# Optimization experiments

Hardware: AMD Instinct MI355X
Metric: run time of the kernel (lower is better)

## Reference

```python
import jax, jax.numpy as jnp
import numpy as np

R = 32  # voxel resolution


def _swish(x):
    return x * jax.nn.sigmoid(x)


def _group_norm(x, gamma, beta, groups, eps=1e-5):
    B, C = x.shape[0], x.shape[1]
    xr = x.reshape(B, groups, -1)
    mean = xr.mean(-1, keepdims=True)
    var = xr.var(-1, keepdims=True)
    xn = ((xr - mean) * jax.lax.rsqrt(var + eps)).reshape(x.shape)
    bshape = (1, C) + (1,) * (x.ndim - 2)
    return xn * gamma.reshape(bshape) + beta.reshape(bshape)


def _conv3d_same(x, w, b):
    # x: [B,C,D,H,W], w: [O,I,k,k,k], SAME padding (k//2)
    k = w.shape[-1]
    p = k // 2
    y = jax.lax.conv_general_dilated(
        x, w, window_strides=(1, 1, 1), padding=[(p, p)] * 3,
        dimension_numbers=('NCDHW', 'OIDHW', 'NCDHW'))
    return y + b[None, :, None, None, None]


def setup_inputs() -> dict:
    key = jax.random.key(0)
    ks = jax.random.split(key, 8)
    B, Cin, Cout, N = 8, 64, 128, 16384
    return {
        'features': jax.random.normal(ks[0], (B, Cin, N), jnp.float32),
        'coords': jax.random.normal(ks[1], (B, 3, N), jnp.float32),
        'temb': jnp.zeros((1,), jnp.float32),
        'w1': jax.random.normal(ks[2], (Cout, Cin, 3, 3, 3), jnp.float32) * 0.02,
        'b1': jnp.zeros((Cout,), jnp.float32),
        'g1_gamma': jnp.ones((Cout,), jnp.float32),
        'g1_beta': jnp.zeros((Cout,), jnp.float32),
        'w2': jax.random.normal(ks[3], (Cout, Cout, 3, 3, 3), jnp.float32) * 0.02,
        'b2': jnp.zeros((Cout,), jnp.float32),
        'g2_gamma': jnp.ones((Cout,), jnp.float32),
        'g2_beta': jnp.zeros((Cout,), jnp.float32),
        'wp': jax.random.normal(ks[4], (Cout, Cin), jnp.float32) * 0.02,
        'bp': jnp.zeros((Cout,), jnp.float32),
        'gp_gamma': jnp.ones((Cout,), jnp.float32),
        'gp_beta': jnp.zeros((Cout,), jnp.float32),
    }


def reference(features, coords, temb, w1, b1, g1_gamma, g1_beta,
              w2, b2, g2_gamma, g2_beta, wp, bp, gp_gamma, gp_beta):
    B, Cin, N = features.shape
    Cout = w1.shape[0]

    # ---- Voxelization (coords are detached in original; no coord grads) ----
    coords_c = jax.lax.stop_gradient(coords)
    nc = coords_c - coords_c.mean(axis=2, keepdims=True)            # [B,3,N]
    nrm = jnp.linalg.norm(nc, axis=1, keepdims=True)                # [B,1,N]
    nc = nc / (nrm.max(axis=2, keepdims=True) * 2.0) + 0.5          # eps=0
    nc = jnp.clip(nc * R, 0.0, R - 1)                               # norm_coords
    vox_idx = jnp.clip(jnp.round(nc).astype(jnp.int32), 0, R - 1)   # [B,3,N]

    flat = (vox_idx[:, 0] * R + vox_idx[:, 1]) * R + vox_idx[:, 2]  # [B,N]
    seg = (flat + jnp.arange(B, dtype=flat.dtype)[:, None] * (R ** 3)).reshape(-1)
    feat_bn = features.transpose(0, 2, 1).reshape(B * N, Cin)       # [B*N,Cin]
    sums = jax.ops.segment_sum(feat_bn, seg, num_segments=B * R ** 3)
    cnts = jax.ops.segment_sum(jnp.ones((B * N,), features.dtype), seg,
                               num_segments=B * R ** 3)
    vox = sums / jnp.maximum(cnts, 1.0)[:, None]                    # avg voxelize
    vox = vox.reshape(B, R, R, R, Cin).transpose(0, 4, 1, 2, 3)     # [B,Cin,R,R,R]

    # ---- Voxel branch: conv3d -> GN -> Swish -> (dropout: eval, no-op) -> conv3d -> GN -> Swish ----
    vox = _swish(_group_norm(_conv3d_same(vox, w1, b1), g1_gamma, g1_beta, 8))
    vox = _swish(_group_norm(_conv3d_same(vox, w2, b2), g2_gamma, g2_beta, 8))

    # ---- Trilinear devoxelize ----
    c = jnp.clip(nc, 0.0, R - 1 - 1e-6)                             # [B,3,N]
    idx0f = jnp.floor(c)
    frac = c - idx0f
    i0 = idx0f.astype(jnp.int32)
    i1 = jnp.minimum(i0 + 1, R - 1)
    vox_flat = vox.reshape(B, Cout, R ** 3)

    def corner(ix, iy, iz):
        fl = (ix * R + iy) * R + iz                                 # [B,N]
        return jnp.take_along_axis(vox_flat, fl[:, None, :], axis=2)  # [B,Cout,N]

    x0, y0, z0 = i0[:, 0], i0[:, 1], i0[:, 2]
    x1, y1, z1 = i1[:, 0], i1[:, 1], i1[:, 2]
    dx = frac[:, 0][:, None, :]
    dy = frac[:, 1][:, None, :]
    dz = frac[:, 2][:, None, :]
    devox = (corner(x0, y0, z0) * (1 - dx) * (1 - dy) * (1 - dz)
             + corner(x0, y0, z1) * (1 - dx) * (1 - dy) * dz
             + corner(x0, y1, z0) * (1 - dx) * dy * (1 - dz)
             + corner(x0, y1, z1) * (1 - dx) * dy * dz
             + corner(x1, y0, z0) * dx * (1 - dy) * (1 - dz)
             + corner(x1, y0, z1) * dx * (1 - dy) * dz
             + corner(x1, y1, z0) * dx * dy * (1 - dz)
             + corner(x1, y1, z1) * dx * dy * dz)                   # [B,Cout,N]

    # ---- Point branch: 1x1 conv1d -> GN(8) -> Swish ----
    pf = jnp.einsum('oc,bcn->bon', wp, features) + bp[None, :, None]
    pf = _swish(_group_norm(pf, gp_gamma, gp_beta, 8))

    fused = devox + pf
    return fused
```

## Files before the change

### kernel.cpp

```cpp
#include <hip/hip_runtime.h>
#include <hip/hip_bf16.h>
#include <cmath>

#define BATCH 8
#define CIN 64
#define COUT 128
#define NPTS 16384
#define RES 32
#define R3 32768
#define NGROUP 8
#define GSIZE 16

typedef __hip_bfloat16 bf16;
typedef __attribute__((ext_vector_type(8))) short short8;
typedef __attribute__((ext_vector_type(4))) float f32x4;

__device__ inline float b2f(ushort u) { union { float f; uint v; } x; x.v = ((uint)u) << 16; return x.f; }
__device__ inline ushort f2bu(float f) { __hip_bfloat16 h = __float2bfloat16(f); return *reinterpret_cast<ushort*>(&h); }

__global__ __launch_bounds__(256) void coord_stats_k(const float* __restrict__ coords,
                                                     float* __restrict__ bstats) {
    int b = blockIdx.x;
    int t = threadIdx.x;
    __shared__ float red[256];
    __shared__ float means[3];
    for (int c = 0; c < 3; ++c) {
        float acc = 0.f;
        const float* p = coords + ((size_t)b * 3 + c) * NPTS;
        for (int n = t; n < NPTS; n += 256) acc += p[n];
        red[t] = acc; __syncthreads();
        for (int s = 128; s > 0; s >>= 1) { if (t < s) red[t] += red[t + s]; __syncthreads(); }
        if (t == 0) means[c] = red[0] * (1.f / NPTS);
        __syncthreads();
    }
    float m0 = means[0], m1 = means[1], m2 = means[2];
    const float* px = coords + ((size_t)b * 3 + 0) * NPTS;
    const float* py = coords + ((size_t)b * 3 + 1) * NPTS;
    const float* pz = coords + ((size_t)b * 3 + 2) * NPTS;
    float mx = 0.f;
    for (int n = t; n < NPTS; n += 256) {
        float dx = px[n] - m0, dy = py[n] - m1, dz = pz[n] - m2;
        mx = fmaxf(mx, sqrtf(dx * dx + dy * dy + dz * dz));
    }
    red[t] = mx; __syncthreads();
    for (int s = 128; s > 0; s >>= 1) { if (t < s) red[t] = fmaxf(red[t], red[t + s]); __syncthreads(); }
    if (t == 0) {
        bstats[b * 4 + 0] = m0; bstats[b * 4 + 1] = m1; bstats[b * 4 + 2] = m2;
        bstats[b * 4 + 3] = 1.f / (2.f * red[0]);
    }
}

__global__ __launch_bounds__(256) void vox_idx_k(const float* __restrict__ coords,
                                                 const float* __restrict__ bstats,
                                                 float4* __restrict__ nc4,
                                                 int* __restrict__ vidx,
                                                 int* __restrict__ slot,
                                                 unsigned int* __restrict__ cnts) {
    int g = blockIdx.x * 256 + threadIdx.x;
    int b = g >> 14, n = g & (NPTS - 1);
    float m0 = bstats[b * 4 + 0], m1 = bstats[b * 4 + 1], m2 = bstats[b * 4 + 2];
    float sc = bstats[b * 4 + 3];
    float x = coords[((size_t)b * 3 + 0) * NPTS + n];
    float y = coords[((size_t)b * 3 + 1) * NPTS + n];
    float z = coords[((size_t)b * 3 + 2) * NPTS + n];
    float ncx = fminf(fmaxf(((x - m0) * sc + 0.5f) * (float)RES, 0.f), RES - 1.f);
    float ncy = fminf(fmaxf(((y - m1) * sc + 0.5f) * (float)RES, 0.f), RES - 1.f);
    float ncz = fminf(fmaxf(((z - m2) * sc + 0.5f) * (float)RES, 0.f), RES - 1.f);
    nc4[g] = make_float4(ncx, ncy, ncz, 0.f);
    int ix = min(max((int)rintf(ncx), 0), RES - 1);
    int iy = min(max((int)rintf(ncy), 0), RES - 1);
    int iz = min(max((int)rintf(ncz), 0), RES - 1);
    int v = b * R3 + (ix * RES + iy) * RES + iz;
    vidx[g] = v;
    slot[g] = (int)atomicAdd(&cnts[v], 1u);
}

__global__ __launch_bounds__(256) void transpose_feats_k(const float* __restrict__ feats,
                                                         bf16* __restrict__ featTb) {
    int blk = blockIdx.x;
    int b = blk >> 8, ntile = blk & 255;
    int t = threadIdx.x;
    __shared__ float lds[64][65];
    for (int e = t; e < 64 * 64; e += 256) {
        int c = e >> 6, n = e & 63;
        lds[c][n] = feats[((size_t)b * CIN + c) * NPTS + ntile * 64 + n];
    }
    __syncthreads();
    for (int e = t; e < 64 * 8; e += 256) {
        int n = e >> 3, oct = e & 7;
        ushort o[8];
#pragma unroll
        for (int j = 0; j < 8; ++j) o[j] = f2bu(lds[oct * 8 + j][n]);
        *(short8*)(featTb + ((((size_t)b << 14) + ntile * 64 + n) * CIN) + oct * 8) = *(short8*)o;
    }
}

__global__ __launch_bounds__(256) void scan1_k(const unsigned int* __restrict__ cnts,
                                               unsigned int* __restrict__ offs,
                                               unsigned int* __restrict__ part) {
    int t = threadIdx.x;
    int g = blockIdx.x * 256 + t;
    unsigned int v = cnts[g];
    __shared__ unsigned int s[256];
    s[t] = v; __syncthreads();
    for (int d = 1; d < 256; d <<= 1) {
        unsigned int x = (t >= d) ? s[t - d] : 0u;
        __syncthreads();
        s[t] += x;
        __syncthreads();
    }
    offs[g] = s[t] - v;
    if (t == 255) part[blockIdx.x] = s[255];
}

__global__ __launch_bounds__(1024) void scan2_k(unsigned int* __restrict__ part) {
    int t = threadIdx.x;
    unsigned int v = part[t];
    __shared__ unsigned int s[1024];
    s[t] = v; __syncthreads();
    for (int d = 1; d < 1024; d <<= 1) {
        unsigned int x = (t >= d) ? s[t - d] : 0u;
        __syncthreads();
        s[t] += x;
        __syncthreads();
    }
    part[t] = s[t] - v;
}

__global__ __launch_bounds__(256) void scan3_k(unsigned int* __restrict__ offs,
                                               const unsigned int* __restrict__ part) {
    int g = blockIdx.x * 256 + threadIdx.x;
    offs[g] += part[blockIdx.x];
}

__global__ __launch_bounds__(256) void scatter_pts_k(const int* __restrict__ vidx,
                                                     const int* __restrict__ slot,
                                                     const unsigned int* __restrict__ offs,
                                                     unsigned int* __restrict__ pidx2) {
    int g = blockIdx.x * 256 + threadIdx.x;
    int v = vidx[g];
    pidx2[offs[v] + slot[g]] = (unsigned int)g;
}

__global__ __launch_bounds__(256) void gather_k(const bf16* __restrict__ featTb,
                                                const unsigned int* __restrict__ cnts,
                                                const unsigned int* __restrict__ offs,
                                                const unsigned int* __restrict__ pidx2,
                                                bf16* __restrict__ voxCL) {
    int u = blockIdx.x * 256 + threadIdx.x;
    int v = u >> 3;
    int l8 = u & 7;
    unsigned int cnt = cnts[v];
    unsigned int off = offs[v];
    float acc[8] = {0.f, 0.f, 0.f, 0.f, 0.f, 0.f, 0.f, 0.f};
    for (unsigned int i = 0; i < cnt; ++i) {
        unsigned int g = pidx2[off + i];
        short8 f = *(const short8*)(featTb + (size_t)g * CIN + l8 * 8);
#pragma unroll
        for (int j = 0; j < 8; ++j) acc[j] += b2f((ushort)f[j]);
    }
    float inv = 1.f / fmaxf((float)cnt, 1.f);
    ushort o[8];
#pragma unroll
    for (int j = 0; j < 8; ++j) o[j] = f2bu(acc[j] * inv);
    *(short8*)(voxCL + (size_t)v * CIN + l8 * 8) = *(short8*)o;
}

template <int CIN_T>
__global__ __launch_bounds__(256) void wreorder_k(const float* __restrict__ w,
                                                  bf16* __restrict__ wf) {
    const int NC = CIN_T / 32;
    int u = blockIdx.x * 256 + threadIdx.x;
    if (u >= 27 * NC * 128 * 4) return;
    int kb = u & 3;
    int co = (u >> 2) & 127;
    int c32 = (u >> 9) % NC;
    int t = u / (512 * NC);
    int cibase = c32 * 32 + kb * 8;
    ushort o[8];
#pragma unroll
    for (int j = 0; j < 8; ++j)
        o[j] = f2bu(w[((size_t)co * CIN_T + cibase + j) * 27 + t]);
    *(short8*)(wf + (size_t)u * 8) = *(short8*)o;
}

__global__ __launch_bounds__(256) void wpreorder_k(const float* __restrict__ wp,
                                                   bf16* __restrict__ wpb) {
    int u = blockIdx.x * 256 + threadIdx.x;
    if (u >= 1024) return;
    int kb = u & 3;
    int co = (u >> 2) & 127;
    int c32 = u >> 9;
    ushort o[8];
#pragma unroll
    for (int j = 0; j < 8; ++j)
        o[j] = f2bu(wp[(size_t)co * CIN + c32 * 32 + kb * 8 + j]);
    *(short8*)(wpb + (size_t)u * 8) = *(short8*)o;
}

template <int CIN_T>
__global__ __launch_bounds__(512, 2) void conv3d_mfma_k(const bf16* __restrict__ x,
                                                        const bf16* __restrict__ wf,
                                                        const float* __restrict__ bias,
                                                        bf16* __restrict__ y,
                                                        float* __restrict__ gnacc) {
    constexpr int NC = CIN_T / 32;
    int blk = blockIdx.x;
    int hq = blk & 7;
    int d = (blk >> 3) & 31;
    int b = blk >> 8;
    int t = threadIdx.x;
    int lane = t & 63;
    int wid = t >> 6;
    int cog = wid >> 1;
    int sg = wid & 1;
    int lr = lane & 15;
    int kb = lane >> 4;

    __shared__ __align__(16) char xs[3 * 6 * 34 * 80];
    __shared__ float gred[8][2];
    if (t < 16) gred[t >> 1][t & 1] = 0.f;

    f32x4 acc[2][4];
#pragma unroll
    for (int r = 0; r < 2; ++r)
#pragma unroll
        for (int j = 0; j < 4; ++j) acc[r][j] = (f32x4){0.f, 0.f, 0.f, 0.f};

    int bbase[4];
#pragma unroll
    for (int j = 0; j < 4; ++j) {
        int sp = sg * 64 + j * 16 + lr;
        int hl = sp >> 5, wl = sp & 31;
        bbase[j] = (hl * 34 + wl) * 80 + kb * 16;
    }

    for (int cc = 0; cc < NC; ++cc) {
        __syncthreads();
        for (int e = t; e < 612 * 4; e += 512) {
            int ekb = e & 3;
            int pos = e >> 2;
            int ww = pos % 34;
            int hh = (pos / 34) % 6;
            int dd = pos / 204;
            int dz = d + dd - 1;
            int hz = hq * 4 + hh - 1;
            int wz = ww - 1;
            short8 v = {0, 0, 0, 0, 0, 0, 0, 0};
            if (dz >= 0 && dz < RES && hz >= 0 && hz < RES && wz >= 0 && wz < RES)
                v = *(const short8*)(x + ((size_t)b * R3 + dz * 1024 + hz * 32 + wz) * CIN_T + cc * 32 + ekb * 8);
            *(short8*)(xs + pos * 80 + ekb * 16) = v;
        }
        __syncthreads();

        const short8* wfp = (const short8*)wf;
        size_t abase = ((size_t)cc * 128 + cog * 32 + lr) * 4 + kb;
#pragma unroll
        for (int dd = 0; dd < 3; ++dd)
#pragma unroll
            for (int dh = 0; dh < 3; ++dh)
#pragma unroll
                for (int dw = 0; dw < 3; ++dw) {
                    int tap = (dd * 3 + dh) * 3 + dw;
                    short8 a0 = wfp[abase + (size_t)tap * NC * 512];
                    short8 a1 = wfp[abase + (size_t)tap * NC * 512 + 64];
                    int toff = ((dd * 6 + dh) * 34 + dw) * 80;
                    short8 bb[4];
#pragma unroll
                    for (int j = 0; j < 4; ++j)
                        bb[j] = *(const short8*)(xs + bbase[j] + toff);
#pragma unroll
                    for (int j = 0; j < 4; ++j) {
                        acc[0][j] = __builtin_amdgcn_mfma_f32_16x16x32_bf16(a0, bb[j], acc[0][j], 0, 0, 0);
                        acc[1][j] = __builtin_amdgcn_mfma_f32_16x16x32_bf16(a1, bb[j], acc[1][j], 0, 0, 0);
                    }
                }
    }

    float sred[2], ssred[2];
#pragma unroll
    for (int r = 0; r < 2; ++r) {
        int co = cog * 32 + r * 16 + kb * 4;
        float4 bv = *(const float4*)(bias + co);
        float s = 0.f, ss = 0.f;
#pragma unroll
        for (int j = 0; j < 4; ++j) {
            int sp = sg * 64 + j * 16 + lr;
            int p = d * 1024 + (hq * 4 + (sp >> 5)) * 32 + (sp & 31);
            float v0 = acc[r][j][0] + bv.x;
            float v1 = acc[r][j][1] + bv.y;
            float v2 = acc[r][j][2] + bv.z;
            float v3 = acc[r][j][3] + bv.w;
            ushort4 o;
            o.x = f2bu(v0); o.y = f2bu(v1); o.z = f2bu(v2); o.w = f2bu(v3);
            *(ushort4*)(y + ((size_t)b * R3 + p) * COUT + co) = o;
            s += v0 + v1 + v2 + v3;
            ss += v0 * v0 + v1 * v1 + v2 * v2 + v3 * v3;
        }
        sred[r] = s; ssred[r] = ss;
    }
#pragma unroll
    for (int m = 1; m < 64; m <<= 1) {
#pragma unroll
        for (int r = 0; r < 2; ++r) {
            sred[r] += __shfl_xor(sred[r], m, 64);
            ssred[r] += __shfl_xor(ssred[r], m, 64);
        }
    }
    if (lane == 0) {
#pragma unroll
        for (int r = 0; r < 2; ++r) {
            atomicAdd(&gred[cog * 2 + r][0], sred[r]);
            atomicAdd(&gred[cog * 2 + r][1], ssred[r]);
        }
    }
    __syncthreads();
    if (t < 16) atomicAdd(&gnacc[(b * 8 + (t >> 1)) * 2 + (t & 1)], gred[t >> 1][t & 1]);
}

__global__ __launch_bounds__(256) void gn_apply_cl_k(bf16* __restrict__ x,
                                                     const float* __restrict__ gnacc,
                                                     const float* __restrict__ gamma,
                                                     const float* __restrict__ beta) {
    int u = blockIdx.x * 256 + threadIdx.x;
    int ci8 = u & 15;
    int p = (u >> 4) & (R3 - 1);
    int b = u >> 19;
    int ci = ci8 * 8;
    int bg = b * 8 + (ci8 >> 1);
    const float M = (float)(GSIZE * R3);
    float s = gnacc[bg * 2], ss = gnacc[bg * 2 + 1];
    float mean = s / M;
    float istd = rsqrtf(fmaxf(ss / M - mean * mean, 0.f) + 1e-5f);
    bf16* ptr = x + ((size_t)b * R3 + p) * COUT + ci;
    short8 v = *(const short8*)ptr;
    ushort o[8];
#pragma unroll
    for (int j = 0; j < 8; ++j) {
        float f = b2f((ushort)v[j]);
        float yv = fmaf((f - mean) * istd, gamma[ci + j], beta[ci + j]);
        o[j] = f2bu(yv / (1.f + __expf(-yv)));
    }
    *(short8*)ptr = *(short8*)o;
}

__global__ __launch_bounds__(256) void pgemm_mfma_k(const bf16* __restrict__ featTb,
                                                    const bf16* __restrict__ wpb,
                                                    const float* __restrict__ bp,
                                                    bf16* __restrict__ pfb,
                                                    float* __restrict__ gnacc) {
    int t = threadIdx.x;
    int lane = t & 63;
    int cog = t >> 6;
    int lr = lane & 15;
    int kb = lane >> 4;
    int g0 = blockIdx.x * 64;
    int b = g0 >> 14;

    __shared__ float gred[8][2];
    if (t < 16) gred[t >> 1][t & 1] = 0.f;
    __syncthreads();

    f32x4 acc[2][4];
#pragma unroll
    for (int r = 0; r < 2; ++r)
#pragma unroll
        for (int j = 0; j < 4; ++j) acc[r][j] = (f32x4){0.f, 0.f, 0.f, 0.f};

    const short8* wfp = (const short8*)wpb;
    const short8* ftp = (const short8*)featTb;
#pragma unroll
    for (int cc = 0; cc < 2; ++cc) {
        size_t abase = ((size_t)cc * 128 + cog * 32 + lr) * 4 + kb;
        short8 a0 = wfp[abase];
        short8 a1 = wfp[abase + 64];
#pragma unroll
        for (int j = 0; j < 4; ++j) {
            short8 bb = ftp[(size_t)(g0 + j * 16 + lr) * 8 + cc * 4 + kb];
            acc[0][j] = __builtin_amdgcn_mfma_f32_16x16x32_bf16(a0, bb, acc[0][j], 0, 0, 0);
            acc[1][j] = __builtin_amdgcn_mfma_f32_16x16x32_bf16(a1, bb, acc[1][j], 0, 0, 0);
        }
    }

    float sred[2], ssred[2];
#pragma unroll
    for (int r = 0; r < 2; ++r) {
        int co = cog * 32 + r * 16 + kb * 4;
        float4 bv = *(const float4*)(bp + co);
        float s = 0.f, ss = 0.f;
#pragma unroll
        for (int j = 0; j < 4; ++j) {
            int g = g0 + j * 16 + lr;
            float v0 = acc[r][j][0] + bv.x;
            float v1 = acc[r][j][1] + bv.y;
            float v2 = acc[r][j][2] + bv.z;
            float v3 = acc[r][j][3] + bv.w;
            ushort4 o;
            o.x = f2bu(v0); o.y = f2bu(v1); o.z = f2bu(v2); o.w = f2bu(v3);
            *(ushort4*)(pfb + (size_t)g * COUT + co) = o;
            s += v0 + v1 + v2 + v3;
            ss += v0 * v0 + v1 * v1 + v2 * v2 + v3 * v3;
        }
        sred[r] = s; ssred[r] = ss;
    }
#pragma unroll
    for (int m = 1; m < 64; m <<= 1) {
#pragma unroll
        for (int r = 0; r < 2; ++r) {
            sred[r] += __shfl_xor(sred[r], m, 64);
            ssred[r] += __shfl_xor(ssred[r], m, 64);
        }
    }
    if (lane == 0) {
#pragma unroll
        for (int r = 0; r < 2; ++r) {
            atomicAdd(&gred[cog * 2 + r][0], sred[r]);
            atomicAdd(&gred[cog * 2 + r][1], ssred[r]);
        }
    }
    __syncthreads();
    if (t < 16) atomicAdd(&gnacc[(b * 8 + (t >> 1)) * 2 + (t & 1)], gred[t >> 1][t & 1]);
}

__global__ __launch_bounds__(256) void fuse2_k(const bf16* __restrict__ vox,
                                               bf16* __restrict__ pfb,
                                               const float4* __restrict__ nc4,
                                               const unsigned int* __restrict__ pidx2,
                                               const float* __restrict__ gn2acc,
                                               const float* __restrict__ gnpacc,
                                               const float* __restrict__ g2g,
                                               const float* __restrict__ g2b,
                                               const float* __restrict__ gpg,
                                               const float* __restrict__ gpb) {
    int t = threadIdx.x;
    int u = blockIdx.x * 256 + t;
    int s = u >> 3;
    int l8 = u & 7;
    unsigned int g = pidx2[s];
    int b = (int)(g >> 14);
    int c0 = l8 * 16;

    const short8* pfp = (const short8*)(pfb + (size_t)g * COUT + c0);
    short8 p0 = pfp[0], p1 = pfp[1];
    float a[16];
#pragma unroll
    for (int j = 0; j < 8; ++j) { a[j] = b2f((ushort)p0[j]); a[8 + j] = b2f((ushort)p1[j]); }

    int bg = b * 8 + l8;
    const float M2 = (float)(GSIZE * R3);
    const float Mp = (float)(GSIZE * NPTS);
    float s2 = gn2acc[bg * 2], ss2 = gn2acc[bg * 2 + 1];
    float mean2 = s2 / M2;
    float istd2 = rsqrtf(fmaxf(ss2 / M2 - mean2 * mean2, 0.f) + 1e-5f);
    float sp = gnpacc[bg * 2], ssp = gnpacc[bg * 2 + 1];
    float meanp = sp / Mp;
    float istdp = rsqrtf(fmaxf(ssp / Mp - meanp * meanp, 0.f) + 1e-5f);
    float ga[16], gb[16];
#pragma unroll
    for (int j = 0; j < 16; ++j) {
        float gm = g2g[c0 + j];
        ga[j] = istd2 * gm;
        gb[j] = g2b[c0 + j] - mean2 * istd2 * gm;
    }

    float4 c4 = nc4[g];
    const float CMAX = (float)(RES - 1) - 1e-6f;
    float cx = fminf(c4.x, CMAX), cy = fminf(c4.y, CMAX), cz = fminf(c4.z, CMAX);
    int ix0 = (int)cx, iy0 = (int)cy, iz0 = (int)cz;
    float fx = cx - ix0, fy = cy - iy0, fz = cz - iz0;
    int ix1 = min(ix0 + 1, RES - 1), iy1 = min(iy0 + 1, RES - 1), iz1 = min(iz0 + 1, RES - 1);
    float gx0 = 1.f - fx, gy0 = 1.f - fy, gz0 = 1.f - fz;
    float wc[8] = {gx0 * gy0 * gz0, gx0 * gy0 * fz, gx0 * fy * gz0, gx0 * fy * fz,
                   fx * gy0 * gz0,  fx * gy0 * fz,  fx * fy * gz0,  fx * fy * fz};
    int fi[8];
    fi[0] = (ix0 * RES + iy0) * RES + iz0; fi[1] = (ix0 * RES + iy0) * RES + iz1;
    fi[2] = (ix0 * RES + iy1) * RES + iz0; fi[3] = (ix0 * RES + iy1) * RES + iz1;
    fi[4] = (ix1 * RES + iy0) * RES + iz0; fi[5] = (ix1 * RES + iy0) * RES + iz1;
    fi[6] = (ix1 * RES + iy1) * RES + iz0; fi[7] = (ix1 * RES + iy1) * RES + iz1;

    const bf16* vb = vox + (size_t)b * R3 * COUT + c0;
    float accv[16] = {0.f, 0.f, 0.f, 0.f, 0.f, 0.f, 0.f, 0.f,
                      0.f, 0.f, 0.f, 0.f, 0.f, 0.f, 0.f, 0.f};
#pragma unroll
    for (int f = 0; f < 8; ++f) {
        const short8* vp = (const short8*)(vb + (size_t)fi[f] * COUT);
        short8 v0 = vp[0], v1 = vp[1];
        float wgt = wc[f];
#pragma unroll
        for (int j = 0; j < 8; ++j) {
            float yv = fmaf(b2f((ushort)v0[j]), ga[j], gb[j]);
            accv[j] = fmaf(wgt, yv / (1.f + __expf(-yv)), accv[j]);
        }
#pragma unroll
        for (int j = 0; j < 8; ++j) {
            float yv = fmaf(b2f((ushort)v1[j]), ga[8 + j], gb[8 + j]);
            accv[8 + j] = fmaf(wgt, yv / (1.f + __expf(-yv)), accv[8 + j]);
        }
    }

    ushort outv[16];
#pragma unroll
    for (int j = 0; j < 16; ++j) {
        float pm = gpg[c0 + j];
        float yv = fmaf((a[j] - meanp) * istdp, pm, gpb[c0 + j]);
        outv[j] = f2bu(yv / (1.f + __expf(-yv)) + accv[j]);
    }
    bf16* pp = pfb + (size_t)g * COUT + c0;
    *(short8*)(pp) = *(short8*)(outv);
    *(short8*)(pp + 8) = *(short8*)(outv + 8);
}

__global__ __launch_bounds__(256) void transpose_out_k(const bf16* __restrict__ pfb,
                                                       float* __restrict__ out) {
    int blk = blockIdx.x;
    int b = blk >> 8, nt = blk & 255;
    int t = threadIdx.x;
    int n0 = nt * 64;
    __shared__ float lds[64][129];
#pragma unroll
    for (int k = 0; k < 4; ++k) {
        int e = t + k * 256;
        int row = e >> 4, oct = e & 15;
        short8 v = *(const short8*)(pfb + (((size_t)b << 14) + n0 + row) * COUT + oct * 8);
#pragma unroll
        for (int j = 0; j < 8; ++j) lds[row][oct * 8 + j] = b2f((ushort)v[j]);
    }
    __syncthreads();
#pragma unroll
    for (int k = 0; k < 32; ++k) {
        int e = t + k * 256;
        int c = e >> 6, n = e & 63;
        out[((size_t)b * COUT + c) * NPTS + n0 + n] = lds[n][c];
    }
}

extern "C" void kernel_launch(void* const* d_in, const int* in_sizes, int n_in,
                              void* d_out, int out_size, void* d_ws, size_t ws_size,
                              hipStream_t stream) {
    const float* features = (const float*)d_in[0];
    const float* coords   = (const float*)d_in[1];
    const float* w1  = (const float*)d_in[3];
    const float* b1  = (const float*)d_in[4];
    const float* g1g = (const float*)d_in[5];
    const float* g1b = (const float*)d_in[6];
    const float* w2  = (const float*)d_in[7];
    const float* b2  = (const float*)d_in[8];
    const float* g2g = (const float*)d_in[9];
    const float* g2b = (const float*)d_in[10];
    const float* wp  = (const float*)d_in[11];
    const float* bp  = (const float*)d_in[12];
    const float* gpg = (const float*)d_in[13];
    const float* gpb = (const float*)d_in[14];
    float* out = (float*)d_out;

    char* ws = (char*)d_ws;
    size_t off = 0;
    bf16* act1 = (bf16*)(ws + off);          off += (size_t)BATCH * R3 * COUT * 2;
    bf16* act2 = (bf16*)(ws + off);          off += (size_t)BATCH * R3 * COUT * 2;
    bf16* voxCL = (bf16*)(ws + off);
    bf16* pfb = (bf16*)(ws + off);           off += (size_t)BATCH * R3 * CIN * 2;
    bf16* featTb = (bf16*)(ws + off);        off += (size_t)BATCH * NPTS * CIN * 2;
    bf16* w1f = (bf16*)(ws + off);           off += (size_t)27 * 2 * 128 * 32 * 2;
    bf16* w2f = (bf16*)(ws + off);           off += (size_t)27 * 4 * 128 * 32 * 2;
    bf16* wpb = (bf16*)(ws + off);           off += (size_t)2 * 128 * 32 * 2;
    float4* nc4 = (float4*)(ws + off);       off += (size_t)BATCH * NPTS * 16;
    unsigned int* cnts = (unsigned int*)(ws + off);  off += (size_t)BATCH * R3 * 4;
    unsigned int* offs = (unsigned int*)(ws + off);  off += (size_t)BATCH * R3 * 4;
    int* vidx = (int*)(ws + off);            off += (size_t)BATCH * NPTS * 4;
    int* slot = (int*)(ws + off);            off += (size_t)BATCH * NPTS * 4;
    unsigned int* pidx2 = (unsigned int*)(ws + off); off += (size_t)BATCH * NPTS * 4;
    unsigned int* part = (unsigned int*)(ws + off);  off += 4096;
    float* bstats = (float*)(ws + off);      off += 256;
    float* gn1acc = (float*)(ws + off);      off += 512;
    float* gn2acc = (float*)(ws + off);      off += 512;
    float* gnpacc = (float*)(ws + off);      off += 512;

    hipMemsetAsync(cnts, 0, (size_t)BATCH * R3 * 4, stream);
    hipMemsetAsync(gn1acc, 0, 3 * 512, stream);

    coord_stats_k<<<BATCH, 256, 0, stream>>>(coords, bstats);
    vox_idx_k<<<BATCH * NPTS / 256, 256, 0, stream>>>(coords, bstats, nc4, vidx, slot, cnts);
    transpose_feats_k<<<BATCH * 256, 256, 0, stream>>>(features, featTb);
    scan1_k<<<BATCH * R3 / 256, 256, 0, stream>>>(cnts, offs, part);
    scan2_k<<<1, 1024, 0, stream>>>(part);
    scan3_k<<<BATCH * R3 / 256, 256, 0, stream>>>(offs, part);
    scatter_pts_k<<<BATCH * NPTS / 256, 256, 0, stream>>>(vidx, slot, offs, pidx2);
    gather_k<<<BATCH * R3 * 8 / 256, 256, 0, stream>>>(featTb, cnts, offs, pidx2, voxCL);

    wreorder_k<CIN><<<(27 * 2 * 128 * 4 + 255) / 256, 256, 0, stream>>>(w1, w1f);
    wreorder_k<COUT><<<(27 * 4 * 128 * 4 + 255) / 256, 256, 0, stream>>>(w2, w2f);
    wpreorder_k<<<4, 256, 0, stream>>>(wp, wpb);

    conv3d_mfma_k<CIN><<<BATCH * 32 * 8, 512, 0, stream>>>(voxCL, w1f, b1, act1, gn1acc);
    gn_apply_cl_k<<<BATCH * R3 * 16 / 256, 256, 0, stream>>>(act1, gn1acc, g1g, g1b);

    conv3d_mfma_k<COUT><<<BATCH * 32 * 8, 512, 0, stream>>>(act1, w2f, b2, act2, gn2acc);

    pgemm_mfma_k<<<BATCH * NPTS / 64, 256, 0, stream>>>(featTb, wpb, bp, pfb, gnpacc);

    fuse2_k<<<BATCH * NPTS * 8 / 256, 256, 0, stream>>>(act2, pfb, nc4, pidx2,
                                                        gn2acc, gnpacc, g2g, g2b, gpg, gpb);

    transpose_out_k<<<BATCH * 256, 256, 0, stream>>>(pfb, out);
}
```

Baseline: 633.5 us.

## Prefetch next input channel chunk into registers during conv3d MFMA loop

Precomputes per-thread global and LDS offsets for the halo tile once, then software-pipelines the channel-chunk loop: the next chunk's global loads go into registers while the current chunk's MFMAs run. The loop is unrolled by two with alternating register buffers. This aims to hide global load latency behind the MFMA work, at the cost of extra registers (two sets of five short8 values plus the offset arrays), which may lower occupancy. The loop assumes an even chunk count, or relies on the cc+1 guard handling an odd count.

```diff
diff --git a/kernel.cpp b/kernel.cpp
--- a/kernel.cpp
+++ b/kernel.cpp
@@ -221,23 +221,12 @@
     __shared__ float gred[8][2];
     if (t < 16) gred[t >> 1][t & 1] = 0.f;
 
-    f32x4 acc[2][4];
-#pragma unroll
-    for (int r = 0; r < 2; ++r)
-#pragma unroll
-        for (int j = 0; j < 4; ++j) acc[r][j] = (f32x4){0.f, 0.f, 0.f, 0.f};
-
-    int bbase[4];
-#pragma unroll
-    for (int j = 0; j < 4; ++j) {
-        int sp = sg * 64 + j * 16 + lr;
-        int hl = sp >> 5, wl = sp & 31;
-        bbase[j] = (hl * 34 + wl) * 80 + kb * 16;
-    }
-
-    for (int cc = 0; cc < NC; ++cc) {
-        __syncthreads();
-        for (int e = t; e < 612 * 4; e += 512) {
+    int goff[5];
+    int laddr[5];
+#pragma unroll
+    for (int i = 0; i < 5; ++i) {
+        int e = t + i * 512;
+        if (e < 612 * 4) {
             int ekb = e & 3;
             int pos = e >> 2;
             int ww = pos % 34;
@@ -246,13 +235,33 @@
             int dz = d + dd - 1;
             int hz = hq * 4 + hh - 1;
             int wz = ww - 1;
-            short8 v = {0, 0, 0, 0, 0, 0, 0, 0};
-            if (dz >= 0 && dz < RES && hz >= 0 && hz < RES && wz >= 0 && wz < RES)
-                v = *(const short8*)(x + ((size_t)b * R3 + dz * 1024 + hz * 32 + wz) * CIN_T + cc * 32 + ekb * 8);
-            *(short8*)(xs + pos * 80 + ekb * 16) = v;
-        }
-        __syncthreads();
-
+            bool ok = (dz >= 0 && dz < RES && hz >= 0 && hz < RES && wz >= 0 && wz < RES);
+            goff[i] = ok ? (int)((((size_t)b * R3 + dz * 1024 + hz * 32 + wz) * CIN_T + ekb * 8) * 2) : -1;
+            laddr[i] = pos * 80 + ekb * 16;
+        } else {
+            goff[i] = -1;
+            laddr[i] = -1;
+        }
+    }
+
+    f32x4 acc[2][4];
+#pragma unroll
+    for (int r = 0; r < 2; ++r)
+#pragma unroll
+        for (int j = 0; j < 4; ++j) acc[r][j] = (f32x4){0.f, 0.f, 0.f, 0.f};
+
+    int bbase[4];
+#pragma unroll
+    for (int j = 0; j < 4; ++j) {
+        int sp = sg * 64 + j * 16 + lr;
+        int hl = sp >> 5, wl = sp & 31;
+        bbase[j] = (hl * 34 + wl) * 80 + kb * 16;
+    }
+
+    const char* xb = (const char*)x;
+    const short8 zero8 = {0, 0, 0, 0, 0, 0, 0, 0};
+
+    auto mfma_chunk = [&](int cc) {
         const short8* wfp = (const short8*)wf;
         size_t abase = ((size_t)cc * 128 + cog * 32 + lr) * 4 + kb;
 #pragma unroll
@@ -275,6 +284,39 @@
                         acc[1][j] = __builtin_amdgcn_mfma_f32_16x16x32_bf16(a1, bb[j], acc[1][j], 0, 0, 0);
                     }
                 }
+    };
+
+    short8 va[5], vb2[5];
+#pragma unroll
+    for (int i = 0; i < 5; ++i) {
+        va[i] = zero8;
+        if (goff[i] >= 0) va[i] = *(const short8*)(xb + goff[i]);
+    }
+
+    for (int cc = 0; cc < NC; cc += 2) {
+        __syncthreads();
+#pragma unroll
+        for (int i = 0; i < 5; ++i)
+            if (laddr[i] >= 0) *(short8*)(xs + laddr[i]) = va[i];
+#pragma unroll
+        for (int i = 0; i < 5; ++i) {
+            vb2[i] = zero8;
+            if (goff[i] >= 0 && cc + 1 < NC) vb2[i] = *(const short8*)(xb + goff[i] + (cc + 1) * 64);
+        }
+        __syncthreads();
+        mfma_chunk(cc);
+
+        __syncthreads();
+#pragma unroll
+        for (int i = 0; i < 5; ++i)
+            if (laddr[i] >= 0) *(short8*)(xs + laddr[i]) = vb2[i];
+#pragma unroll
+        for (int i = 0; i < 5; ++i) {
+            va[i] = zero8;
+            if (goff[i] >= 0 && cc + 2 < NC) va[i] = *(const short8*)(xb + goff[i] + (cc + 2) * 64);
+        }
+        __syncthreads();
+        mfma_chunk(cc + 1);
     }
 
     float sred[2], ssred[2];
```

New measurement: 693.6 us. 9.5% more time.
